# Kernel tuning notes

Measured on AMD Instinct MI355X. Metric: run time of the kernel, lower is better.

The kernel has to match this reference:

```python
import jax, jax.numpy as jnp
import numpy as np
from functools import partial

N_NODES = 100000
N_EDGES = 1600000
N_LABEL = 200000
D = 128


def _add_self_loops(edge_index, edge_weight, num_nodes):
    # PyG GCNConv default: add self loops with fill_value = 1.0
    loops = jnp.arange(num_nodes, dtype=edge_index.dtype)
    src = jnp.concatenate([edge_index[0], loops])
    dst = jnp.concatenate([edge_index[1], loops])
    ew = jnp.concatenate([edge_weight, jnp.ones((num_nodes,), edge_weight.dtype)])
    return src, dst, ew


def _gcn_norm(src, dst, ew, num_nodes):
    # symmetric normalization: D^-1/2 A D^-1/2, degrees over target index
    deg = jax.ops.segment_sum(ew, dst, num_segments=num_nodes)
    dinv = jnp.where(deg > 0, jax.lax.rsqrt(deg), 0.0)
    return dinv[src] * ew * dinv[dst]


def _gcn_conv(x, W, b, src, dst, norm, num_nodes):
    h = x @ W                      # [N, D] small GEMM
    msg = h[src] * norm[:, None]   # gather + scale, [E+N, D]
    out = jax.ops.segment_sum(msg, dst, num_segments=num_nodes)
    return out + b


def setup_inputs() -> dict:
    key = jax.random.key(0)
    ks = jax.random.split(key, 10)
    s = 1.0 / np.sqrt(D)
    return {
        "x": jax.random.normal(ks[0], (N_NODES, D), jnp.float32),
        "edge_index": jax.random.randint(ks[1], (2, N_EDGES), 0, N_NODES, jnp.int64),
        "edge_weight": jax.random.uniform(ks[2], (N_EDGES,), jnp.float32),
        "edge_label_index": jax.random.randint(ks[3], (2, N_LABEL), 0, N_NODES, jnp.int64),
        "W1": jax.random.uniform(ks[4], (D, D), jnp.float32, -s, s),
        "b1": jnp.zeros((D,), jnp.float32),
        "W2": jax.random.uniform(ks[5], (D, D), jnp.float32, -s, s),
        "b2": jnp.zeros((D,), jnp.float32),
        "lin_W": jax.random.uniform(ks[6], (D, D), jnp.float32, -s, s),
        "lin_b": jax.random.uniform(ks[7], (D,), jnp.float32, -s, s),
    }


def reference(x, edge_index, edge_weight, edge_label_index, W1, b1, W2, b2, lin_W, lin_b):
    n = x.shape[0]
    src, dst, ew = _add_self_loops(edge_index, edge_weight, n)
    norm = _gcn_norm(src, dst, ew, n)
    out = jax.nn.relu(_gcn_conv(x, W1, b1, src, dst, norm, n))
    out = jax.nn.relu(_gcn_conv(out, W2, b2, src, dst, norm, n))
    had = out[edge_label_index[0]] * out[edge_label_index[1]]  # [EL, D]
    # lin then sum over features == had @ lin_W @ 1 + sum(lin_b)
    return jnp.sum(had @ lin_W + lin_b, axis=-1)
```

## Files before the change

kernel.cpp:

```cpp
#include <hip/hip_runtime.h>

#define N_NODES 100000
#define N_EDGES 1600000
#define N_LABEL 200000
#define D 128

#define SCAN_BLOCKS ((N_NODES + 255) / 256)

typedef __attribute__((ext_vector_type(8))) short short8;
typedef __attribute__((ext_vector_type(4))) float f32x4;

static __device__ __forceinline__ unsigned short f2bf(float f) {
    unsigned u = __float_as_uint(f);
    u += 0x7fffu + ((u >> 16) & 1u);
    return (unsigned short)(u >> 16);
}
static __device__ __forceinline__ float bf2f_lo(unsigned p) {
    return __uint_as_float(p << 16);
}
static __device__ __forceinline__ float bf2f_hi(unsigned p) {
    return __uint_as_float(p & 0xffff0000u);
}

__global__ void k_prep(const float* __restrict__ linW, const float* __restrict__ linb,
                       float* __restrict__ wv, float* __restrict__ cval) {
    int t = threadIdx.x;
    float s = 0.f;
    for (int j = 0; j < D; ++j) s += linW[t * D + j];
    wv[t] = s;
    __shared__ float red[128];
    red[t] = linb[t];
    __syncthreads();
    for (int st = 64; st > 0; st >>= 1) {
        if (t < st) red[t] += red[t + st];
        __syncthreads();
    }
    if (t == 0) *cval = red[0];
}

__global__ void k_prepw(const float* __restrict__ W, unsigned short* __restrict__ Wt) {
    int i = blockIdx.x * 256 + threadIdx.x;
    if (i < D * D) {
        int k = i >> 7, n = i & 127;
        Wt[n * D + k] = f2bf(W[i]);
    }
}

__global__ void k_init(int* __restrict__ offs) {
    int i = blockIdx.x * 256 + threadIdx.x;
    if (i < N_NODES + 4) offs[i] = 0;
}

__global__ void k_count(const int* __restrict__ ei, int* __restrict__ cnt,
                        int* __restrict__ rank) {
    int e = blockIdx.x * 256 + threadIdx.x;
    if (e < N_EDGES) rank[e] = atomicAdd(&cnt[ei[N_EDGES + e]], 1);
}

__global__ void k_scan1(int* __restrict__ offs, int* __restrict__ bsum) {
    __shared__ int sm[256];
    int tid = threadIdx.x;
    int i = blockIdx.x * 256 + tid;
    int v = (i < N_NODES) ? offs[i] : 0;
    sm[tid] = v;
    __syncthreads();
    for (int st = 1; st < 256; st <<= 1) {
        int add = (tid >= st) ? sm[tid - st] : 0;
        __syncthreads();
        sm[tid] += add;
        __syncthreads();
    }
    if (i < N_NODES) offs[i] = sm[tid] - v;
    if (tid == 255) bsum[blockIdx.x] = sm[255];
}

__global__ void k_scan2(int* __restrict__ bsum) {
    __shared__ int sm[512];
    int tid = threadIdx.x;
    int v = (tid < SCAN_BLOCKS) ? bsum[tid] : 0;
    sm[tid] = v;
    __syncthreads();
    for (int st = 1; st < 512; st <<= 1) {
        int add = (tid >= st) ? sm[tid - st] : 0;
        __syncthreads();
        sm[tid] += add;
        __syncthreads();
    }
    if (tid < SCAN_BLOCKS) bsum[tid] = sm[tid] - v;
}

__global__ void k_scan3(int* __restrict__ offs, const int* __restrict__ bsum) {
    int i = blockIdx.x * 256 + threadIdx.x;
    if (i < N_NODES) offs[i] += bsum[i >> 8];
    if (i == 0) offs[N_NODES] = N_EDGES;
}

__global__ void k_scatter(const int* __restrict__ ei, const float* __restrict__ ew,
                          const int* __restrict__ offs, const int* __restrict__ rank,
                          int2* __restrict__ csr) {
    int e = blockIdx.x * 256 + threadIdx.x;
    if (e < N_EDGES) {
        int d = ei[N_EDGES + e];
        int pos = offs[d] + rank[e];
        csr[pos] = make_int2(ei[e] << 6, __float_as_int(ew[e]));
    }
}

__global__ void k_degdinv(const int* __restrict__ offs, const int2* __restrict__ csr,
                          float* __restrict__ dinv) {
    int i = blockIdx.x * 256 + threadIdx.x;
    if (i < N_NODES) {
        int p0 = offs[i], p1 = offs[i + 1];
        float s = 1.0f;
        for (int p = p0; p < p1; ++p) s += __int_as_float(csr[p].y);
        dinv[i] = rsqrtf(s);
    }
}

template <bool IN_F32>
__global__ __launch_bounds__(256) void k_gemm(const void* __restrict__ INp,
                                              const unsigned short* __restrict__ Wt,
                                              const float* __restrict__ dinv,
                                              unsigned short* __restrict__ H) {
    __shared__ unsigned short xs[64 * 128];
    __shared__ unsigned short wts[128 * 128];
    int tid = threadIdx.x;
    int rowBase = blockIdx.x * 64;

#pragma unroll
    for (int i = 0; i < 4; ++i) {
        int idx = tid + i * 256;
        int r = idx >> 4;
        int kc = (idx & 15) << 3;
        int gr = rowBase + r;
        uint4 pk = make_uint4(0, 0, 0, 0);
        if (gr < N_NODES) {
            if (IN_F32) {
                const float* X = (const float*)INp;
                float4 v0 = *(const float4*)&X[(size_t)gr * D + kc];
                float4 v1 = *(const float4*)&X[(size_t)gr * D + kc + 4];
                pk.x = (unsigned)f2bf(v0.x) | ((unsigned)f2bf(v0.y) << 16);
                pk.y = (unsigned)f2bf(v0.z) | ((unsigned)f2bf(v0.w) << 16);
                pk.z = (unsigned)f2bf(v1.x) | ((unsigned)f2bf(v1.y) << 16);
                pk.w = (unsigned)f2bf(v1.z) | ((unsigned)f2bf(v1.w) << 16);
            } else {
                pk = *(const uint4*)&((const unsigned short*)INp)[(size_t)gr * D + kc];
            }
        }
        *(uint4*)&xs[(r * D + kc) ^ ((r & 7) << 3)] = pk;
    }
#pragma unroll
    for (int i = 0; i < 8; ++i) {
        int idx = tid + i * 256;
        int n = idx >> 4;
        int kc = (idx & 15) << 3;
        uint4 pk = *(const uint4*)&Wt[n * D + kc];
        *(uint4*)&wts[(n * D + kc) ^ ((n & 7) << 3)] = pk;
    }
    __syncthreads();

    int lane = tid & 63;
    int wrow = (tid >> 6) * 16;
    int l15 = lane & 15;
    int l4 = (lane >> 4) << 2;

    f32x4 acc[8] = {};
    union FragU { short8 v; uint2 u2[2]; };

#pragma unroll
    for (int kk = 0; kk < 4; ++kk) {
        int kb = kk * 32 + l4;
        int m = wrow + l15;
        FragU a;
        a.u2[0] = *(uint2*)&xs[(m * D + kb) ^ ((m & 7) << 3)];
        a.u2[1] = *(uint2*)&xs[(m * D + kb + 16) ^ ((m & 7) << 3)];
#pragma unroll
        for (int ct = 0; ct < 8; ++ct) {
            int n = ct * 16 + l15;
            FragU b;
            b.u2[0] = *(uint2*)&wts[(n * D + kb) ^ ((n & 7) << 3)];
            b.u2[1] = *(uint2*)&wts[(n * D + kb + 16) ^ ((n & 7) << 3)];
            acc[ct] = __builtin_amdgcn_mfma_f32_16x16x32_bf16(a.v, b.v, acc[ct], 0, 0, 0);
        }
    }

    int rloc = wrow + l4;
    float dn[4];
#pragma unroll
    for (int r = 0; r < 4; ++r) {
        int gr = rowBase + rloc + r;
        dn[r] = (gr < N_NODES) ? dinv[gr] : 0.f;
    }
#pragma unroll
    for (int ct = 0; ct < 8; ++ct) {
#pragma unroll
        for (int r = 0; r < 4; ++r) {
            int gr = rowBase + rloc + r;
            if (gr < N_NODES)
                H[(size_t)gr * D + ct * 16 + l15] = f2bf(acc[ct][r] * dn[r]);
        }
    }
}

__global__ __launch_bounds__(256) void k_agg(const unsigned* __restrict__ h,
                                             const float* __restrict__ dinv,
                                             const int* __restrict__ offs,
                                             const int2* __restrict__ csr,
                                             const float* __restrict__ bias,
                                             unsigned* __restrict__ out) {
    int wid = threadIdx.x >> 6;
    int lane = threadIdx.x & 63;
    int node = blockIdx.x * 4 + wid;
    if (node >= N_NODES) return;

    int eh = lane >> 5;
    int fl = lane & 31;

    float a0 = 0.f, a1 = 0.f, a2 = 0.f, a3 = 0.f;
    int p0 = offs[node], p1 = offs[node + 1];

    for (int p = p0; p < p1; p += 16) {
        int2 cc[8];
        float ww[8];
#pragma unroll
        for (int k = 0; k < 8; ++k) {
            int pe = p + (k << 1) + eh;
            bool v = pe < p1;
            cc[k] = csr[v ? pe : p0];
            ww[k] = v ? __int_as_float(cc[k].y) : 0.f;
        }
        uint2 hh[8];
#pragma unroll
        for (int k = 0; k < 8; ++k)
            hh[k] = *(const uint2*)&h[(size_t)(unsigned)cc[k].x + fl * 2];
#pragma unroll
        for (int k = 0; k < 8; ++k) {
            a0 += ww[k] * bf2f_lo(hh[k].x);
            a1 += ww[k] * bf2f_hi(hh[k].x);
            a2 += ww[k] * bf2f_lo(hh[k].y);
            a3 += ww[k] * bf2f_hi(hh[k].y);
        }
    }

    a0 += __shfl_xor(a0, 32, 64);
    a1 += __shfl_xor(a1, 32, 64);
    a2 += __shfl_xor(a2, 32, 64);
    a3 += __shfl_xor(a3, 32, 64);

    if (eh == 0) {
        uint2 sv = *(const uint2*)&h[(size_t)node * 64 + fl * 2];
        a0 += bf2f_lo(sv.x);
        a1 += bf2f_hi(sv.x);
        a2 += bf2f_lo(sv.y);
        a3 += bf2f_hi(sv.y);
        float dn = dinv[node];
        float4 bb = *(const float4*)&bias[fl * 4];
        a0 = fmaxf(a0 * dn + bb.x, 0.f);
        a1 = fmaxf(a1 * dn + bb.y, 0.f);
        a2 = fmaxf(a2 * dn + bb.z, 0.f);
        a3 = fmaxf(a3 * dn + bb.w, 0.f);
        uint2 o;
        o.x = (unsigned)f2bf(a0) | ((unsigned)f2bf(a1) << 16);
        o.y = (unsigned)f2bf(a2) | ((unsigned)f2bf(a3) << 16);
        *(uint2*)&out[(size_t)node * 64 + fl * 2] = o;
    }
}

__global__ void k_final(const int* __restrict__ eli, const unsigned* __restrict__ o2,
                        const float* __restrict__ wv, const float* __restrict__ cval,
                        float* __restrict__ res) {
    unsigned g = blockIdx.x * 256 + threadIdx.x;
    int l = g >> 6;
    int t = g & 63;
    if (l < N_LABEL) {
        int a = eli[l];
        int b = eli[N_LABEL + l];
        unsigned ua = o2[(size_t)a * 64 + t];
        unsigned ub = o2[(size_t)b * 64 + t];
        float2 w2 = *(const float2*)&wv[t * 2];
        float s = bf2f_lo(ua) * bf2f_lo(ub) * w2.x + bf2f_hi(ua) * bf2f_hi(ub) * w2.y;
#pragma unroll
        for (int st = 32; st > 0; st >>= 1) s += __shfl_down(s, st, 64);
        if (t == 0) res[l] = s + *cval;
    }
}

extern "C" void kernel_launch(void* const* d_in, const int* in_sizes, int n_in,
                              void* d_out, int out_size, void* d_ws, size_t ws_size,
                              hipStream_t stream) {
    const float* x    = (const float*)d_in[0];
    const int*   ei   = (const int*)d_in[1];
    const float* ew   = (const float*)d_in[2];
    const int*   eli  = (const int*)d_in[3];
    const float* W1   = (const float*)d_in[4];
    const float* b1   = (const float*)d_in[5];
    const float* W2   = (const float*)d_in[6];
    const float* b2   = (const float*)d_in[7];
    const float* linW = (const float*)d_in[8];
    const float* linb = (const float*)d_in[9];
    float* res = (float*)d_out;

    float*          ws    = (float*)d_ws;
    float*          dinv  = ws;
    int*            offs  = (int*)(dinv + N_NODES);
    int*            bsum  = offs + N_NODES + 4;
    int2*           csr   = (int2*)(bsum + 512);
    unsigned*       h_bf  = (unsigned*)(csr + N_EDGES);
    unsigned*       agg   = h_bf + (size_t)N_NODES * 64;
    unsigned*       out2  = agg + (size_t)N_NODES * 64;
    float*          wv    = (float*)(out2 + (size_t)N_NODES * 64);
    float*          cval  = wv + D;
    unsigned short* w1t   = (unsigned short*)(cval + 1);
    unsigned short* w2t   = w1t + D * D;
    int*            rank  = (int*)agg;

    k_prep<<<1, 128, 0, stream>>>(linW, linb, wv, cval);
    k_prepw<<<64, 256, 0, stream>>>(W1, w1t);
    k_prepw<<<64, 256, 0, stream>>>(W2, w2t);

    k_init<<<(N_NODES + 4 + 255) / 256, 256, 0, stream>>>(offs);
    k_count<<<(N_EDGES + 255) / 256, 256, 0, stream>>>(ei, offs, rank);
    k_scan1<<<SCAN_BLOCKS, 256, 0, stream>>>(offs, bsum);
    k_scan2<<<1, 512, 0, stream>>>(bsum);
    k_scan3<<<SCAN_BLOCKS, 256, 0, stream>>>(offs, bsum);
    k_scatter<<<(N_EDGES + 255) / 256, 256, 0, stream>>>(ei, ew, offs, rank, csr);
    k_degdinv<<<(N_NODES + 255) / 256, 256, 0, stream>>>(offs, csr, dinv);

    const int GB = (N_NODES + 63) / 64;

    k_gemm<true><<<GB, 256, 0, stream>>>(x, w1t, dinv, (unsigned short*)h_bf);
    k_agg<<<(N_NODES + 3) / 4, 256, 0, stream>>>(h_bf, dinv, offs, csr, b1, agg);

    k_gemm<false><<<GB, 256, 0, stream>>>(agg, w2t, dinv, (unsigned short*)h_bf);
    k_agg<<<(N_NODES + 3) / 4, 256, 0, stream>>>(h_bf, dinv, offs, csr, b2, out2);

    k_final<<<(N_LABEL * 64 + 255) / 256, 256, 0, stream>>>(eli, out2, wv, cval, res);
}
```

Measured before the change: 373.1 us.

## Split CSR degree counters into 8 partitions and widen aggregation batch

Degree counting now spreads atomics over 8 per-partition counter arrays chosen by block index. This is meant to reduce contention on popular destination nodes. The scan step sums the partitions and builds per-partition offsets that the scatter uses. The aggregation kernel also processes 32 edges per iteration instead of 16, putting more gathers in flight at the cost of more registers. The extra counter arrays add init and scan traffic and make CSR order within a node depend on the partition.

Result: no change. 378.9 us (+1.5%).

```diff
diff --git a/kernel.cpp b/kernel.cpp
--- a/kernel.cpp
+++ b/kernel.cpp
@@ -46,22 +46,28 @@
     }
 }
 
-__global__ void k_init(int* __restrict__ offs) {
+__global__ void k_init(int* __restrict__ cnt8) {
     int i = blockIdx.x * 256 + threadIdx.x;
-    if (i < N_NODES + 4) offs[i] = 0;
-}
-
-__global__ void k_count(const int* __restrict__ ei, int* __restrict__ cnt,
+    if (i < 8 * N_NODES) cnt8[i] = 0;
+}
+
+__global__ void k_count(const int* __restrict__ ei, int* __restrict__ cnt8,
                         int* __restrict__ rank) {
     int e = blockIdx.x * 256 + threadIdx.x;
-    if (e < N_EDGES) rank[e] = atomicAdd(&cnt[ei[N_EDGES + e]], 1);
-}
-
-__global__ void k_scan1(int* __restrict__ offs, int* __restrict__ bsum) {
+    int p = blockIdx.x & 7;
+    if (e < N_EDGES) rank[e] = atomicAdd(&cnt8[p * N_NODES + ei[N_EDGES + e]], 1);
+}
+
+__global__ void k_scan1(const int* __restrict__ cnt8, int* __restrict__ offs,
+                        int* __restrict__ bsum) {
     __shared__ int sm[256];
     int tid = threadIdx.x;
     int i = blockIdx.x * 256 + tid;
-    int v = (i < N_NODES) ? offs[i] : 0;
+    int v = 0;
+    if (i < N_NODES) {
+#pragma unroll
+        for (int q = 0; q < 8; ++q) v += cnt8[q * N_NODES + i];
+    }
     sm[tid] = v;
     __syncthreads();
     for (int st = 1; st < 256; st <<= 1) {
@@ -89,19 +95,29 @@
     if (tid < SCAN_BLOCKS) bsum[tid] = sm[tid] - v;
 }
 
-__global__ void k_scan3(int* __restrict__ offs, const int* __restrict__ bsum) {
+__global__ void k_scan3(int* __restrict__ offs, const int* __restrict__ bsum,
+                        const int* __restrict__ cnt8, int* __restrict__ pofs) {
     int i = blockIdx.x * 256 + threadIdx.x;
-    if (i < N_NODES) offs[i] += bsum[i >> 8];
+    if (i < N_NODES) {
+        int base = offs[i] + bsum[i >> 8];
+        offs[i] = base;
+#pragma unroll
+        for (int q = 0; q < 8; ++q) {
+            pofs[q * N_NODES + i] = base;
+            base += cnt8[q * N_NODES + i];
+        }
+    }
     if (i == 0) offs[N_NODES] = N_EDGES;
 }
 
 __global__ void k_scatter(const int* __restrict__ ei, const float* __restrict__ ew,
-                          const int* __restrict__ offs, const int* __restrict__ rank,
+                          const int* __restrict__ pofs, const int* __restrict__ rank,
                           int2* __restrict__ csr) {
     int e = blockIdx.x * 256 + threadIdx.x;
+    int p = blockIdx.x & 7;
     if (e < N_EDGES) {
         int d = ei[N_EDGES + e];
-        int pos = offs[d] + rank[e];
+        int pos = pofs[p * N_NODES + d] + rank[e];
         csr[pos] = make_int2(ei[e] << 6, __float_as_int(ew[e]));
     }
 }
@@ -219,22 +235,22 @@
     float a0 = 0.f, a1 = 0.f, a2 = 0.f, a3 = 0.f;
     int p0 = offs[node], p1 = offs[node + 1];
 
-    for (int p = p0; p < p1; p += 16) {
-        int2 cc[8];
-        float ww[8];
-#pragma unroll
-        for (int k = 0; k < 8; ++k) {
+    for (int p = p0; p < p1; p += 32) {
+        int2 cc[16];
+        float ww[16];
+#pragma unroll
+        for (int k = 0; k < 16; ++k) {
             int pe = p + (k << 1) + eh;
             bool v = pe < p1;
             cc[k] = csr[v ? pe : p0];
             ww[k] = v ? __int_as_float(cc[k].y) : 0.f;
         }
-        uint2 hh[8];
-#pragma unroll
-        for (int k = 0; k < 8; ++k)
+        uint2 hh[16];
+#pragma unroll
+        for (int k = 0; k < 16; ++k)
             hh[k] = *(const uint2*)&h[(size_t)(unsigned)cc[k].x + fl * 2];
 #pragma unroll
-        for (int k = 0; k < 8; ++k) {
+        for (int k = 0; k < 16; ++k) {
             a0 += ww[k] * bf2f_lo(hh[k].x);
             a1 += ww[k] * bf2f_hi(hh[k].x);
             a2 += ww[k] * bf2f_lo(hh[k].y);
@@ -304,7 +320,9 @@
     float*          dinv  = ws;
     int*            offs  = (int*)(dinv + N_NODES);
     int*            bsum  = offs + N_NODES + 4;
-    int2*           csr   = (int2*)(bsum + 512);
+    int*            cnt8  = bsum + 512;
+    int*            pofs  = cnt8 + 8 * N_NODES;
+    int2*           csr   = (int2*)(pofs + 8 * N_NODES);
     unsigned*       h_bf  = (unsigned*)(csr + N_EDGES);
     unsigned*       agg   = h_bf + (size_t)N_NODES * 64;
     unsigned*       out2  = agg + (size_t)N_NODES * 64;
@@ -318,12 +336,12 @@
     k_prepw<<<64, 256, 0, stream>>>(W1, w1t);
     k_prepw<<<64, 256, 0, stream>>>(W2, w2t);
 
-    k_init<<<(N_NODES + 4 + 255) / 256, 256, 0, stream>>>(offs);
-    k_count<<<(N_EDGES + 255) / 256, 256, 0, stream>>>(ei, offs, rank);
-    k_scan1<<<SCAN_BLOCKS, 256, 0, stream>>>(offs, bsum);
+    k_init<<<(8 * N_NODES + 255) / 256, 256, 0, stream>>>(cnt8);
+    k_count<<<(N_EDGES + 255) / 256, 256, 0, stream>>>(ei, cnt8, rank);
+    k_scan1<<<SCAN_BLOCKS, 256, 0, stream>>>(cnt8, offs, bsum);
     k_scan2<<<1, 512, 0, stream>>>(bsum);
-    k_scan3<<<SCAN_BLOCKS, 256, 0, stream>>>(offs, bsum);
-    k_scatter<<<(N_EDGES + 255) / 256, 256, 0, stream>>>(ei, ew, offs, rank, csr);
+    k_scan3<<<SCAN_BLOCKS, 256, 0, stream>>>(offs, bsum, cnt8, pofs);
+    k_scatter<<<(N_EDGES + 255) / 256, 256, 0, stream>>>(ei, ew, pofs, rank, csr);
     k_degdinv<<<(N_NODES + 255) / 256, 256, 0, stream>>>(offs, csr, dinv);
 
     const int GB = (N_NODES + 63) / 64;
```
